# Performance work log

Measured on AMD Instinct MI355X. Metric: run time of the kernel, lower is better.

Reference implementation:

```python
import jax, jax.numpy as jnp
import numpy as np

D_MODEL = 1024
NUM_HEADS = 16
ROPE_THETA = 10000.0


def setup_inputs() -> dict:
    key = jax.random.key(0)
    ks = jax.random.split(key, 5)
    B, S, D = 4, 2048, D_MODEL
    scale = 1.0 / np.sqrt(D)
    return {
        "x": jax.random.normal(ks[0], (B, S, D), dtype=jnp.float32),
        "Wq": jax.random.normal(ks[1], (D, D), dtype=jnp.float32) * scale,
        "Wk": jax.random.normal(ks[2], (D, D), dtype=jnp.float32) * scale,
        "Wv": jax.random.normal(ks[3], (D, D), dtype=jnp.float32) * scale,
        "Wo": jax.random.normal(ks[4], (D, D), dtype=jnp.float32) * scale,
        "token_positions": jnp.arange(S, dtype=jnp.int32),
    }


def _rope(x, pos, theta=ROPE_THETA):
    # x: (b, h, s, d); interleaved-pair rotary embedding
    d = x.shape[-1]
    inv_freq = 1.0 / (theta ** (jnp.arange(0, d, 2, dtype=jnp.float32) / d))  # (d/2,)
    ang = pos.astype(jnp.float32)[:, None] * inv_freq[None, :]  # (s, d/2)
    cos, sin = jnp.cos(ang), jnp.sin(ang)
    x1, x2 = x[..., ::2], x[..., 1::2]
    out = jnp.stack([x1 * cos - x2 * sin, x1 * sin + x2 * cos], axis=-1)
    return out.reshape(x.shape)


def reference(x, Wq, Wk, Wv, Wo, token_positions):
    B, S, D = x.shape
    H = NUM_HEADS
    dh = D // H
    # torch nn.Linear(bias=False): y = x @ W.T
    q = jnp.einsum('bsd,ed->bse', x, Wq).reshape(B, S, H, dh).transpose(0, 2, 1, 3)
    k = jnp.einsum('bsd,ed->bse', x, Wk).reshape(B, S, H, dh).transpose(0, 2, 1, 3)
    v = jnp.einsum('bsd,ed->bse', x, Wv).reshape(B, S, H, dh).transpose(0, 2, 1, 3)
    q = _rope(q, token_positions)
    k = _rope(k, token_positions)
    scores = jnp.einsum('bhqd,bhkd->bhqk', q, k) / jnp.sqrt(jnp.array(dh, x.dtype))
    causal = jnp.tril(jnp.ones((S, S), dtype=bool))
    scores = jnp.where(causal, scores, jnp.array(-jnp.inf, scores.dtype))
    probs = jax.nn.softmax(scores, axis=-1)
    attn = jnp.einsum('bhqk,bhkd->bhqd', probs, v)  # (b, h, s, dh)
    attn = attn.transpose(0, 2, 1, 3).reshape(B, S, D)
    return jnp.einsum('bsd,ed->bse', attn, Wo)
```

## Files before the change

### kernel.cpp

```cpp
#include <hip/hip_runtime.h>
#include <hip/hip_bf16.h>
#include <stdint.h>

#define S_LEN 2048
#define BATCH 4
#define NH    16
#define DH    64
#define DM    1024
#define MTOT  (BATCH*S_LEN)

typedef short bf16x8 __attribute__((ext_vector_type(8)));
typedef float f32x4 __attribute__((ext_vector_type(4)));
typedef uint32_t u32x4 __attribute__((ext_vector_type(4)));

__device__ __forceinline__ uint16_t f2bf(float f) {
  union { float f; uint32_t i; } c; c.f = f;
  uint32_t r = c.i + 0x7fffu + ((c.i >> 16) & 1u);
  return (uint16_t)(r >> 16);
}
__device__ __forceinline__ float bf2f(uint16_t u) {
  union { uint32_t i; float f; } c; c.i = ((uint32_t)u) << 16; return c.f;
}

__device__ __forceinline__ uint32_t cvt_pk_bf16(float a, float b) {
  uint32_t r;
  asm("v_cvt_pk_bf16_f32 %0, %1, %2" : "=v"(r) : "v"(a), "v"(b));
  return r;
}

__device__ __forceinline__ void async_copy16(void* lds, const void* g) {
  __builtin_amdgcn_global_load_lds(
      (const __attribute__((address_space(1))) void*)g,
      (__attribute__((address_space(3))) void*)lds, 16, 0, 0);
}

__global__ __launch_bounds__(256) void cvt_f32_bf16(const float* __restrict__ in,
                                                    uint16_t* __restrict__ out, int n4) {
  int stride = gridDim.x * blockDim.x;
  for (int i = blockIdx.x * blockDim.x + threadIdx.x; i < n4; i += stride) {
    float4 v = ((const float4*)in)[i];
    ushort4 o;
    o.x = f2bf(v.x); o.y = f2bf(v.y); o.z = f2bf(v.z); o.w = f2bf(v.w);
    ((ushort4*)out)[i] = o;
  }
}

__global__ __launch_bounds__(256) void cvt_w4(const float* __restrict__ wq,
                                              const float* __restrict__ wk,
                                              const float* __restrict__ wv,
                                              const float* __restrict__ wo,
                                              uint16_t* __restrict__ out) {
  const int sel = blockIdx.y;
  const float* src = sel == 0 ? wq : sel == 1 ? wk : sel == 2 ? wv : wo;
  uint16_t* dst = out + (size_t)sel * DM * DM;
  const int n4 = DM * DM / 4;
  const int stride = gridDim.x * blockDim.x;
  for (int i = blockIdx.x * blockDim.x + threadIdx.x; i < n4; i += stride) {
    float4 v = ((const float4*)src)[i];
    ushort4 o;
    o.x = f2bf(v.x); o.y = f2bf(v.y); o.z = f2bf(v.z); o.w = f2bf(v.w);
    ((ushort4*)dst)[i] = o;
  }
}

template<int MODE>
__global__ __launch_bounds__(512) void gemm_bt(const uint16_t* __restrict__ A,
                                               const uint16_t* __restrict__ Bw,
                                               void* __restrict__ outp,
                                               const int* __restrict__ pos) {
  constexpr int K = DM;
  constexpr int NT = K / 64;
  __shared__ __align__(16) uint16_t lA[2][128 * 64];
  __shared__ __align__(16) uint16_t lB[2][256 * 64];
  const int tid = threadIdx.x;
  const int w = tid >> 6, lane = tid & 63;
  const int l15 = lane & 15, lhi = lane >> 4;
  const int wr = w >> 2, wc = w & 3;

  const int nx = gridDim.x, nwg = nx * gridDim.y;
  const int flat = blockIdx.y * nx + blockIdx.x;
  const int wg = (flat & 7) * (nwg >> 3) + (flat >> 3);
  const int bm = (wg / nx) * 128, bn = (wg % nx) * 256;

  auto stage = [&](int b, int t) {
    const int k0 = t * 64;
#pragma unroll
    for (int j = 0; j < 2; ++j) {
      const int c = j * 512 + tid;
      const int row = c >> 3, cir = c & 7;
      const int gc = cir ^ (row & 7);
      async_copy16((char*)lA[b] + c * 16,
                   (const char*)A + ((size_t)(bm + row) * K + k0 + gc * 8) * 2);
    }
#pragma unroll
    for (int j = 0; j < 4; ++j) {
      const int c = j * 512 + tid;
      const int row = c >> 3, cir = c & 7;
      const int gc = cir ^ (row & 7);
      async_copy16((char*)lB[b] + c * 16,
                   (const char*)Bw + ((size_t)(bn + row) * K + k0 + gc * 8) * 2);
    }
  };

  f32x4 acc[4][4] = {};

  stage(0, 0);
  __syncthreads();

  int cur = 0;
  for (int t = 0; t < NT; ++t) {
    if (t + 1 < NT) stage(cur ^ 1, t + 1);

    bf16x8 af[4][2], bfr[4][2];
#pragma unroll
    for (int mf = 0; mf < 4; ++mf) {
      const int ar = wr * 64 + mf * 16 + l15;
#pragma unroll
      for (int kc = 0; kc < 2; ++kc)
        af[mf][kc] = *(const bf16x8*)((const char*)lA[cur] + ar * 128 +
                                      (((kc * 4 + lhi) ^ (ar & 7)) << 4));
    }
#pragma unroll
    for (int nf = 0; nf < 4; ++nf) {
      const int br = wc * 64 + nf * 16 + l15;
#pragma unroll
      for (int kc = 0; kc < 2; ++kc)
        bfr[nf][kc] = *(const bf16x8*)((const char*)lB[cur] + br * 128 +
                                       (((kc * 4 + lhi) ^ (br & 7)) << 4));
    }
    __builtin_amdgcn_s_setprio(1);
#pragma unroll
    for (int mf = 0; mf < 4; ++mf)
#pragma unroll
      for (int nf = 0; nf < 4; ++nf)
#pragma unroll
        for (int kc = 0; kc < 2; ++kc)
          acc[mf][nf] = __builtin_amdgcn_mfma_f32_16x16x32_bf16(
              af[mf][kc], bfr[nf][kc], acc[mf][nf], 0, 0, 0);
    __builtin_amdgcn_s_setprio(0);

    __syncthreads();
    cur ^= 1;
  }

  if (MODE == 0) {
    const int tsel = bn >> 10;
    uint16_t* out = (uint16_t*)outp + (size_t)tsel * ((size_t)MTOT * DM);
    if (tsel < 2) {
      const float l2t_32 = 0.41524101186092074f;
      const float qsc = tsel == 0 ? 0.18033688011112042f : 1.0f;
#pragma unroll
      for (int mf = 0; mf < 4; ++mf) {
        float ps[4];
#pragma unroll
        for (int r = 0; r < 4; ++r) {
          const int m = bm + wr * 64 + mf * 16 + lhi * 4 + r;
          ps[r] = (float)pos[m & (S_LEN - 1)];
        }
#pragma unroll
        for (int nf = 0; nf < 4; ++nf) {
          const int n = bn + wc * 64 + nf * 16 + l15;
          const int e = n & 1023;
          const int h = e >> 6, d = e & 63;
          const float inv = __builtin_amdgcn_exp2f(-(float)(d >> 1) * l2t_32);
#pragma unroll
          for (int r = 0; r < 4; ++r) {
            const int m = bm + wr * 64 + mf * 16 + lhi * 4 + r;
            const int b = m >> 11, s = m & (S_LEN - 1);
            const float v = acc[mf][nf][r];
            const float p = __shfl_xor(v, 1);
            const float ang = ps[r] * inv;
            const float cs = __cosf(ang) * qsc, sn = __sinf(ang) * qsc;
            const float val = (l15 & 1) ? (p * sn + v * cs) : (v * cs - p * sn);
            out[(((size_t)(b * NH + h) * S_LEN + s) << 6) + d] = f2bf(val);
          }
        }
      }
    } else {
#pragma unroll
      for (int mf = 0; mf < 4; ++mf)
#pragma unroll
        for (int nf = 0; nf < 4; ++nf)
#pragma unroll
          for (int r = 0; r < 4; ++r) {
            const int m = bm + wr * 64 + mf * 16 + lhi * 4 + r;
            const int n = bn + wc * 64 + nf * 16 + l15;
            const int b = m >> 11, s = m & (S_LEN - 1);
            const int e = n & 1023;
            const int h = e >> 6, d = e & 63;
            out[(((size_t)(b * NH + h) * S_LEN + s) << 6) + d] = f2bf(acc[mf][nf][r]);
          }
    }
  } else {
    float* out = (float*)outp;
#pragma unroll
    for (int mf = 0; mf < 4; ++mf)
#pragma unroll
      for (int nf = 0; nf < 4; ++nf)
#pragma unroll
        for (int r = 0; r < 4; ++r) {
          const int m = bm + wr * 64 + mf * 16 + lhi * 4 + r;
          const int n = bn + wc * 64 + nf * 16 + l15;
          out[(size_t)m * DM + n] = acc[mf][nf][r];
        }
  }
}

__global__ __launch_bounds__(256) void transpose_v(const uint16_t* __restrict__ v,
                                                   uint16_t* __restrict__ vt) {
  __shared__ uint16_t t[64 * 65];
  const int bh = blockIdx.y, s0 = blockIdx.x * 64;
  const uint16_t* vb = v + (size_t)bh * S_LEN * 64 + (size_t)s0 * 64;
  uint16_t* ob = vt + (size_t)bh * 64 * S_LEN + s0;
  for (int o = threadIdx.x; o < 64 * 64; o += 256) {
    const int r = o >> 6, c = o & 63;
    t[c * 65 + r] = vb[(size_t)r * 64 + c];
  }
  __syncthreads();
  for (int o = threadIdx.x; o < 64 * 64; o += 256) {
    const int d = o >> 6, p = o & 63;
    const int sp = (p & 32) | (((p >> 2) & 3) << 3) | (((p >> 4) & 1) << 2) | (p & 3);
    ob[(size_t)d * S_LEN + sp] = t[d * 65 + p];
  }
}

__global__ __launch_bounds__(512, 4) void attn_kernel(const uint16_t* __restrict__ q,
                                                      const uint16_t* __restrict__ kk,
                                                      const uint16_t* __restrict__ vt,
                                                      uint16_t* __restrict__ o) {
  const int bh = blockIdx.y;
  const int p = blockIdx.x;
  const int tid = threadIdx.x;
  const int w = __builtin_amdgcn_readfirstlane(tid >> 6);
  const int lane = tid & 63;
  const int l15 = lane & 15, lhi = lane >> 4;
  const uint16_t* qb = q + (size_t)bh * S_LEN * DH;
  const uint16_t* kb = kk + (size_t)bh * S_LEN * DH;
  const uint16_t* vb = vt + (size_t)bh * DH * S_LEN;

  __shared__ uint16_t lK[2][128 * 64];
  __shared__ uint16_t lV[2][64 * 128];

  const int krow_l = lane >> 3;
  const int scK = (lane & 7) ^ krow_l;
  const int vrow_l = lane >> 4;

  auto stage = [&](int b, int t) {
    const int k0 = t * 128;
#pragma unroll
    for (int i = 0; i < 2; ++i) {
      const int krow = w * 16 + i * 8 + krow_l;
      async_copy16((char*)lK[b] + w * 2048 + i * 1024 + lane * 16,
                   (const char*)kb + ((size_t)(k0 + krow) * 64 + scK * 8) * 2);
      const int vd = w * 8 + i * 4 + vrow_l;
      const int scV = (lane & 15) ^ (vd & 15);
      async_copy16((char*)lV[b] + w * 2048 + i * 1024 + lane * 16,
                   (const char*)vb + ((size_t)vd * S_LEN + k0 + scV * 8) * 2);
    }
  };

  stage(0, 0);
  asm volatile("s_waitcnt vmcnt(0)" ::: "memory");
  __syncthreads();

  int cur = 0;
  const int b_out = bh >> 4, h_out = bh & 15;

  for (int s = 0; s < 2; ++s) {
    const int qtile = s ? p : (15 - p);
    const int q0 = qtile * 128 + w * 16;

    bf16x8 qf[2];
#pragma unroll
    for (int c = 0; c < 2; ++c)
      qf[c] = *(const bf16x8*)(qb + (size_t)(q0 + l15) * DH + c * 32 + lhi * 8);

    f32x4 oa[4] = {};
    float mr = -1e30f, lr = 0.f;

    const int nt = qtile + 1;
    for (int t = 0; t < nt; ++t) {
      if (t + 1 < nt) stage(cur ^ 1, t + 1);
      else if (s == 0) stage(cur ^ 1, 0);

      const bool diag = (t == qtile);
      const int fMf = diag ? w : 7;
      const int fE  = diag ? (w | 1) : 7;
      const int cE  = diag ? (w >> 1) : 3;

      f32x4 sf[8];
      __builtin_amdgcn_s_setprio(1);
#pragma unroll
      for (int f = 0; f < 8; ++f) {
        f32x4 z = {0.f, 0.f, 0.f, 0.f};
        if (f <= fMf) {
          const int kr = f * 16 + l15;
          const char* kbase = (const char*)lK[cur] + kr * 128;
          bf16x8 kf0 = *(const bf16x8*)(kbase + ((lhi ^ (kr & 7)) << 4));
          bf16x8 kf1 = *(const bf16x8*)(kbase + (((4 + lhi) ^ (kr & 7)) << 4));
          z = __builtin_amdgcn_mfma_f32_16x16x32_bf16(kf0, qf[0], z, 0, 0, 0);
          z = __builtin_amdgcn_mfma_f32_16x16x32_bf16(kf1, qf[1], z, 0, 0, 0);
        }
        sf[f] = z;
      }
      __builtin_amdgcn_s_setprio(0);

      if (diag) {
        const int qrow = q0 + l15;
        const int k0 = t * 128;
#pragma unroll
        for (int f = 0; f < 8; ++f)
          if (f <= fE)
#pragma unroll
            for (int r = 0; r < 4; ++r) {
              const int kv = k0 + f * 16 + lhi * 4 + r;
              if (kv > qrow) sf[f][r] = -1e30f;
            }
      }

      float pm = -1e30f;
#pragma unroll
      for (int f = 0; f < 8; ++f)
        if (f <= fE)
#pragma unroll
          for (int r = 0; r < 4; ++r) pm = fmaxf(pm, sf[f][r]);
      pm = fmaxf(pm, __shfl_xor(pm, 16));
      pm = fmaxf(pm, __shfl_xor(pm, 32));

      if (!__all(pm <= mr + 8.0f)) {
        const float mn = fmaxf(mr, pm);
        const float resc = __builtin_amdgcn_exp2f(mr - mn);
        mr = mn;
        lr *= resc;
#pragma unroll
        for (int r = 0; r < 4; ++r) {
          const float rb = __shfl(resc, (lhi << 2) + r);
#pragma unroll
          for (int df = 0; df < 4; ++df) oa[df][r] *= rb;
        }
      }

      float rs = 0.f;
#pragma unroll
      for (int f = 0; f < 8; ++f)
        if (f <= fE)
#pragma unroll
          for (int r = 0; r < 4; ++r) {
            const float pv = __builtin_amdgcn_exp2f(sf[f][r] - mr);
            sf[f][r] = pv;
            rs += pv;
          }
      rs += __shfl_xor(rs, 16);
      rs += __shfl_xor(rs, 32);
      lr += rs;

#pragma unroll
      for (int c = 0; c < 4; ++c) {
        if (c <= cE) {
          u32x4 u;
          u.x = cvt_pk_bf16(sf[2 * c][0], sf[2 * c][1]);
          u.y = cvt_pk_bf16(sf[2 * c][2], sf[2 * c][3]);
          u.z = cvt_pk_bf16(sf[2 * c + 1][0], sf[2 * c + 1][1]);
          u.w = cvt_pk_bf16(sf[2 * c + 1][2], sf[2 * c + 1][3]);
          bf16x8 pa = __builtin_bit_cast(bf16x8, u);
          __builtin_amdgcn_s_setprio(1);
#pragma unroll
          for (int df = 0; df < 4; ++df) {
            const int vr = df * 16 + l15;
            bf16x8 vf = *(const bf16x8*)((const char*)lV[cur] + vr * 256 +
                                         ((((c << 2) + lhi) ^ (vr & 15)) << 4));
            oa[df] = __builtin_amdgcn_mfma_f32_16x16x32_bf16(pa, vf, oa[df], 0, 0, 0);
          }
          __builtin_amdgcn_s_setprio(0);
        }
      }

      asm volatile("s_waitcnt vmcnt(0)" ::: "memory");
      __syncthreads();
      cur ^= 1;
    }

    float inv[4];
#pragma unroll
    for (int r = 0; r < 4; ++r)
      inv[r] = __builtin_amdgcn_rcpf(__shfl(lr, (lhi << 2) + r));
#pragma unroll
    for (int df = 0; df < 4; ++df)
#pragma unroll
      for (int r = 0; r < 4; ++r) {
        const int srow_o = q0 + lhi * 4 + r;
        const float val = oa[df][r] * inv[r];
        const int d = df * 16 + l15;
        o[((size_t)(b_out * S_LEN + srow_o)) * DM + h_out * 64 + d] = f2bf(val);
      }
  }
}

extern "C" void kernel_launch(void* const* d_in, const int* in_sizes, int n_in,
                              void* d_out, int out_size, void* d_ws, size_t ws_size,
                              hipStream_t stream) {
  const float* x = (const float*)d_in[0];
  const float* Wq = (const float*)d_in[1];
  const float* Wk = (const float*)d_in[2];
  const float* Wv = (const float*)d_in[3];
  const float* Wo = (const float*)d_in[4];
  const int* pos = (const int*)d_in[5];

  char* ws = (char*)d_ws;
  size_t off = 0;
  auto alloc = [&](size_t bytes) {
    void* p = ws + off;
    off += (bytes + 255) & ~(size_t)255;
    return p;
  };
  uint16_t* xb    = (uint16_t*)alloc((size_t)MTOT * DM * 2);
  uint16_t* wqkvb = (uint16_t*)alloc((size_t)4 * DM * DM * 2);
  uint16_t* qkvb  = (uint16_t*)alloc((size_t)3 * MTOT * DM * 2);
  uint16_t* vtb   = (uint16_t*)alloc((size_t)MTOT * DM * 2);
  uint16_t* wob = wqkvb + (size_t)3 * DM * DM;
  uint16_t* qb = qkvb;
  uint16_t* kbuf = qkvb + (size_t)MTOT * DM;
  uint16_t* vbuf = qkvb + (size_t)2 * MTOT * DM;
  uint16_t* attnb = xb;

  cvt_f32_bf16<<<2048, 256, 0, stream>>>(x, xb, MTOT * DM / 4);
  cvt_w4<<<dim3(128, 4), 256, 0, stream>>>(Wq, Wk, Wv, Wo, wqkvb);

  gemm_bt<0><<<dim3(12, MTOT / 128), 512, 0, stream>>>(xb, wqkvb, qkvb, pos);

  transpose_v<<<dim3(32, 64), 256, 0, stream>>>(vbuf, vtb);

  attn_kernel<<<dim3(8, 64), 512, 0, stream>>>(qb, kbuf, vtb, attnb);

  gemm_bt<1><<<dim3(4, MTOT / 128), 512, 0, stream>>>(attnb, wob, d_out, nullptr);
}
```

Baseline: 178.1 us.

## Replace GEMM with 256x256 tile, 8-phase interleaved load/MFMA pipeline

Rewrites the projection GEMM to use 256x256 block tiles with 8 waves each owning a 128x64 output region. K-slices of 32 are staged as separate LDS slots, and global-to-LDS copies are interleaved with MFMA phases under explicit vmcnt waits and barriers. The goal is more data reuse per block and better overlap of memory with compute. In exchange it uses more accumulator registers, halves the grid size, and drops the XOR swizzle, which may bring LDS bank conflicts.

```diff
diff --git a/kernel.cpp b/kernel.cpp
--- a/kernel.cpp
+++ b/kernel.cpp
@@ -64,14 +64,13 @@
 }
 
 template<int MODE>
-__global__ __launch_bounds__(512) void gemm_bt(const uint16_t* __restrict__ A,
-                                               const uint16_t* __restrict__ Bw,
-                                               void* __restrict__ outp,
-                                               const int* __restrict__ pos) {
+__global__ __launch_bounds__(512, 2) void gemm8p(const uint16_t* __restrict__ Aa,
+                                                 const uint16_t* __restrict__ Bw,
+                                                 void* __restrict__ outp,
+                                                 const int* __restrict__ pos) {
   constexpr int K = DM;
-  constexpr int NT = K / 64;
-  __shared__ __align__(16) uint16_t lA[2][128 * 64];
-  __shared__ __align__(16) uint16_t lB[2][256 * 64];
+  __shared__ __align__(16) uint16_t sA[2][2][256 * 32];
+  __shared__ __align__(16) uint16_t sB[2][2][256 * 32];
   const int tid = threadIdx.x;
   const int w = tid >> 6, lane = tid & 63;
   const int l15 = lane & 15, lhi = lane >> 4;
@@ -80,67 +79,82 @@
   const int nx = gridDim.x, nwg = nx * gridDim.y;
   const int flat = blockIdx.y * nx + blockIdx.x;
   const int wg = (flat & 7) * (nwg >> 3) + (flat >> 3);
-  const int bm = (wg / nx) * 128, bn = (wg % nx) * 256;
-
-  auto stage = [&](int b, int t) {
-    const int k0 = t * 64;
-#pragma unroll
-    for (int j = 0; j < 2; ++j) {
-      const int c = j * 512 + tid;
-      const int row = c >> 3, cir = c & 7;
-      const int gc = cir ^ (row & 7);
-      async_copy16((char*)lA[b] + c * 16,
-                   (const char*)A + ((size_t)(bm + row) * K + k0 + gc * 8) * 2);
+  const int bm = (wg / nx) * 256, bn = (wg % nx) * 256;
+
+  const int r0 = tid >> 2;
+  const int c0 = (tid & 3) * 8;
+
+  auto stageA = [&](int par, int kc, int tt) {
+    const int kk = tt * 64 + kc * 32;
+#pragma unroll
+    for (int j = 0; j < 2; ++j)
+      async_copy16((char*)sA + ((par * 2 + kc) * 1024 + j * 512 + tid) * 16,
+                   (const char*)Aa + ((size_t)(bm + j * 128 + r0) * K + kk + c0) * 2);
+  };
+  auto stageB = [&](int par, int kc, int tt) {
+    const int kk = tt * 64 + kc * 32;
+#pragma unroll
+    for (int j = 0; j < 2; ++j)
+      async_copy16((char*)sB + ((par * 2 + kc) * 1024 + j * 512 + tid) * 16,
+                   (const char*)Bw + ((size_t)(bn + j * 128 + r0) * K + kk + c0) * 2);
+  };
+
+  f32x4 acc[8][4] = {};
+
+  stageA(0, 0, 0); stageB(0, 0, 0);
+  stageA(0, 1, 0); stageB(0, 1, 0);
+  stageA(1, 0, 1); stageB(1, 0, 1);
+  asm volatile("s_waitcnt vmcnt(6)" ::: "memory");
+  __builtin_amdgcn_s_barrier();
+
+  constexpr int NIT = K / 128;
+  for (int it = 0; it < NIT; ++it) {
+    const int base = 2 * it;
+    bf16x8 bfr[4];
+#pragma unroll
+    for (int p = 0; p < 8; ++p) {
+      const int t2 = p >> 2, kc = (p >> 1) & 1, mh = p & 1;
+
+      asm volatile("s_waitcnt vmcnt(6)" ::: "memory");
+      __builtin_amdgcn_sched_barrier(0);
+
+      bf16x8 af[4];
+      const char* slotA = (const char*)&sA[t2][kc][0];
+#pragma unroll
+      for (int mf = 0; mf < 4; ++mf)
+        af[mf] = *(const bf16x8*)(slotA + (wr * 128 + mh * 64 + mf * 16 + l15) * 64 + lhi * 16);
+      if (mh == 0) {
+        const char* slotB = (const char*)&sB[t2][kc][0];
+#pragma unroll
+        for (int nf = 0; nf < 4; ++nf)
+          bfr[nf] = *(const bf16x8*)(slotB + (wc * 64 + nf * 16 + l15) * 64 + lhi * 16);
+      }
+
+      {
+        int tt;
+        switch (p) {
+          case 0: tt = base + 1; if (tt > 15) tt = 15; stageA(1, 1, tt); break;
+          case 1: tt = base + 1; if (tt > 15) tt = 15; stageB(1, 1, tt); break;
+          case 2: tt = base + 2; if (tt > 15) tt = 15; stageA(0, 0, tt); break;
+          case 3: tt = base + 2; if (tt > 15) tt = 15; stageB(0, 0, tt); break;
+          case 4: tt = base + 2; if (tt > 15) tt = 15; stageA(0, 1, tt); break;
+          case 5: tt = base + 2; if (tt > 15) tt = 15; stageB(0, 1, tt); break;
+          case 6: tt = base + 3; if (tt > 15) tt = 15; stageA(1, 0, tt); break;
+          default: tt = base + 3; if (tt > 15) tt = 15; stageB(1, 0, tt); break;
+        }
+      }
+
+      __builtin_amdgcn_s_barrier();
+      __builtin_amdgcn_s_setprio(1);
+#pragma unroll
+      for (int mf = 0; mf < 4; ++mf)
+#pragma unroll
+        for (int nf = 0; nf < 4; ++nf)
+          acc[mh * 4 + mf][nf] = __builtin_amdgcn_mfma_f32_16x16x32_bf16(
+              af[mf], bfr[nf], acc[mh * 4 + mf][nf], 0, 0, 0);
+      __builtin_amdgcn_s_setprio(0);
+      __builtin_amdgcn_s_barrier();
     }
-#pragma unroll
-    for (int j = 0; j < 4; ++j) {
-      const int c = j * 512 + tid;
-      const int row = c >> 3, cir = c & 7;
-      const int gc = cir ^ (row & 7);
-      async_copy16((char*)lB[b] + c * 16,
-                   (const char*)Bw + ((size_t)(bn + row) * K + k0 + gc * 8) * 2);
-    }
-  };
-
-  f32x4 acc[4][4] = {};
-
-  stage(0, 0);
-  __syncthreads();
-
-  int cur = 0;
-  for (int t = 0; t < NT; ++t) {
-    if (t + 1 < NT) stage(cur ^ 1, t + 1);
-
-    bf16x8 af[4][2], bfr[4][2];
-#pragma unroll
-    for (int mf = 0; mf < 4; ++mf) {
-      const int ar = wr * 64 + mf * 16 + l15;
-#pragma unroll
-      for (int kc = 0; kc < 2; ++kc)
-        af[mf][kc] = *(const bf16x8*)((const char*)lA[cur] + ar * 128 +
-                                      (((kc * 4 + lhi) ^ (ar & 7)) << 4));
-    }
-#pragma unroll
-    for (int nf = 0; nf < 4; ++nf) {
-      const int br = wc * 64 + nf * 16 + l15;
-#pragma unroll
-      for (int kc = 0; kc < 2; ++kc)
-        bfr[nf][kc] = *(const bf16x8*)((const char*)lB[cur] + br * 128 +
-                                       (((kc * 4 + lhi) ^ (br & 7)) << 4));
-    }
-    __builtin_amdgcn_s_setprio(1);
-#pragma unroll
-    for (int mf = 0; mf < 4; ++mf)
-#pragma unroll
-      for (int nf = 0; nf < 4; ++nf)
-#pragma unroll
-        for (int kc = 0; kc < 2; ++kc)
-          acc[mf][nf] = __builtin_amdgcn_mfma_f32_16x16x32_bf16(
-              af[mf][kc], bfr[nf][kc], acc[mf][nf], 0, 0, 0);
-    __builtin_amdgcn_s_setprio(0);
-
-    __syncthreads();
-    cur ^= 1;
   }
 
   if (MODE == 0) {
@@ -150,11 +164,12 @@
       const float l2t_32 = 0.41524101186092074f;
       const float qsc = tsel == 0 ? 0.18033688011112042f : 1.0f;
 #pragma unroll
-      for (int mf = 0; mf < 4; ++mf) {
+      for (int mfi = 0; mfi < 8; ++mfi) {
+        const int mo = (mfi >> 2) * 64 + (mfi & 3) * 16;
         float ps[4];
 #pragma unroll
         for (int r = 0; r < 4; ++r) {
-          const int m = bm + wr * 64 + mf * 16 + lhi * 4 + r;
+          const int m = bm + wr * 128 + mo + lhi * 4 + r;
           ps[r] = (float)pos[m & (S_LEN - 1)];
         }
 #pragma unroll
@@ -165,44 +180,48 @@
           const float inv = __builtin_amdgcn_exp2f(-(float)(d >> 1) * l2t_32);
 #pragma unroll
           for (int r = 0; r < 4; ++r) {
-            const int m = bm + wr * 64 + mf * 16 + lhi * 4 + r;
+            const int m = bm + wr * 128 + mo + lhi * 4 + r;
             const int b = m >> 11, s = m & (S_LEN - 1);
-            const float v = acc[mf][nf][r];
-            const float p = __shfl_xor(v, 1);
+            const float v = acc[mfi][nf][r];
+            const float pr = __shfl_xor(v, 1);
             const float ang = ps[r] * inv;
             const float cs = __cosf(ang) * qsc, sn = __sinf(ang) * qsc;
-            const float val = (l15 & 1) ? (p * sn + v * cs) : (v * cs - p * sn);
+            const float val = (l15 & 1) ? (pr * sn + v * cs) : (v * cs - pr * sn);
             out[(((size_t)(b * NH + h) * S_LEN + s) << 6) + d] = f2bf(val);
           }
         }
       }
     } else {
 #pragma unroll
-      for (int mf = 0; mf < 4; ++mf)
+      for (int mfi = 0; mfi < 8; ++mfi) {
+        const int mo = (mfi >> 2) * 64 + (mfi & 3) * 16;
 #pragma unroll
         for (int nf = 0; nf < 4; ++nf)
 #pragma unroll
           for (int r = 0; r < 4; ++r) {
-            const int m = bm + wr * 64 + mf * 16 + lhi * 4 + r;
+            const int m = bm + wr * 128 + mo + lhi * 4 + r;
             const int n = bn + wc * 64 + nf * 16 + l15;
             const int b = m >> 11, s = m & (S_LEN - 1);
             const int e = n & 1023;
             const int h = e >> 6, d = e & 63;
-            out[(((size_t)(b * NH + h) * S_LEN + s) << 6) + d] = f2bf(acc[mf][nf][r]);
+            out[(((size_t)(b * NH + h) * S_LEN + s) << 6) + d] = f2bf(acc[mfi][nf][r]);
           }
+      }
     }
   } else {
     float* out = (float*)outp;
 #pragma unroll
-    for (int mf = 0; mf < 4; ++mf)
+    for (int mfi = 0; mfi < 8; ++mfi) {
+      const int mo = (mfi >> 2) * 64 + (mfi & 3) * 16;
 #pragma unroll
       for (int nf = 0; nf < 4; ++nf)
 #pragma unroll
         for (int r = 0; r < 4; ++r) {
-          const int m = bm + wr * 64 + mf * 16 + lhi * 4 + r;
+          const int m = bm + wr * 128 + mo + lhi * 4 + r;
           const int n = bn + wc * 64 + nf * 16 + l15;
-          out[(size_t)m * DM + n] = acc[mf][nf][r];
-        }
+          out[(size_t)m * DM + n] = acc[mfi][nf][r];
+        }
+    }
   }
 }
 
@@ -426,11 +445,11 @@
   cvt_f32_bf16<<<2048, 256, 0, stream>>>(x, xb, MTOT * DM / 4);
   cvt_w4<<<dim3(128, 4), 256, 0, stream>>>(Wq, Wk, Wv, Wo, wqkvb);
 
-  gemm_bt<0><<<dim3(12, MTOT / 128), 512, 0, stream>>>(xb, wqkvb, qkvb, pos);
+  gemm8p<0><<<dim3(12, MTOT / 256), 512, 0, stream>>>(xb, wqkvb, qkvb, pos);
 
   transpose_v<<<dim3(32, 64), 256, 0, stream>>>(vbuf, vtb);
 
   attn_kernel<<<dim3(8, 64), 512, 0, stream>>>(qb, kbuf, vtb, attnb);
 
-  gemm_bt<1><<<dim3(4, MTOT / 128), 512, 0, stream>>>(attnb, wob, d_out, nullptr);
-}
+  gemm8p<1><<<dim3(4, MTOT / 256), 512, 0, stream>>>(attnb, wob, d_out, nullptr);
+}
```

Result: slower. 190.0 us (+6.7%).
